# Performance work log

Hardware: AMD Instinct MI355X
Metric: run time of the kernel (lower is better)

Reference implementation:

```python
import jax, jax.numpy as jnp
import numpy as np

NH = 12
RD = 16  # partial RoPE dim


def setup_inputs() -> dict:
    key = jax.random.key(0)
    k1, k2, k3 = jax.random.split(key, 3)
    B, T, C = 4, 2048, 768
    x = jax.random.normal(k1, (B, T, C), dtype=jnp.float32)
    w_qkv = jax.random.normal(k2, (3 * C, C), dtype=jnp.float32) * 0.02
    w_out = jax.random.normal(k3, (C, C), dtype=jnp.float32) * 0.02
    return {"x": x, "w_qkv": w_qkv, "w_out": w_out}


def _rope_tables(T, dtype):
    freqs = 1.0 / (10000.0 ** (jnp.arange(0, RD, 2, dtype=jnp.float32) / RD))
    f = jnp.arange(T, dtype=jnp.float32)[:, None] * freqs[None, :]  # [T, RD//2]
    cos = jnp.cos(f)[None, None].astype(dtype)  # [1,1,T,RD//2]
    sin = jnp.sin(f)[None, None].astype(dtype)
    return cos, sin


def _rope(t, cos, sin):
    # t: [B, H, T, hd]; rotate only the first RD dims (split-half style)
    r, p = t[..., :RD], t[..., RD:]
    r1, r2 = r[..., : RD // 2], r[..., RD // 2 :]
    rot = jnp.concatenate([r1 * cos - r2 * sin, r2 * cos + r1 * sin], axis=-1)
    return jnp.concatenate([rot, p], axis=-1)


def reference(x, w_qkv, w_out):
    B, T, C = x.shape
    hd = C // NH
    qkv = jnp.einsum('btc,dc->btd', x, w_qkv).reshape(B, T, 3, NH, hd)
    q, k, v = (jnp.transpose(qkv[:, :, i], (0, 2, 1, 3)) for i in range(3))  # [B,H,T,hd]
    cos, sin = _rope_tables(T, x.dtype)
    q = _rope(q, cos, sin)
    k = _rope(k, cos, sin)
    scale = 1.0 / np.sqrt(hd).astype(np.float32)
    scores = jnp.einsum('bhqd,bhkd->bhqk', q, k) * scale  # [B,H,T,T]
    causal = jnp.tril(jnp.ones((T, T), dtype=bool))
    scores = jnp.where(causal[None, None], scores, jnp.finfo(scores.dtype).min)
    attn = jax.nn.softmax(scores, axis=-1)
    o = jnp.einsum('bhqk,bhkd->bhqd', attn, v)  # [B,H,T,hd]
    o = jnp.transpose(o, (0, 2, 1, 3)).reshape(B, T, C)
    return jnp.einsum('btc,dc->btd', o, w_out)
```

## Files before the change

### kernel.cpp

```cpp
#include <hip/hip_runtime.h>
#include <math.h>


namespace {

constexpr int B_ = 4, T_ = 2048, C_ = 768, NH_ = 12, HD_ = 64;
constexpr int BH_ = B_ * NH_;
constexpr size_t QS_ = (size_t)BH_ * T_ * HD_;

typedef short short8 __attribute__((ext_vector_type(8)));
typedef float f32x4 __attribute__((ext_vector_type(4)));

__device__ inline ushort f2bf(float f) {
    unsigned u = __builtin_bit_cast(unsigned, f);
    u += 0x7fff + ((u >> 16) & 1);
    return (ushort)(u >> 16);
}
__device__ inline float bf2f(ushort h) {
    unsigned u = (unsigned)h << 16;
    return __builtin_bit_cast(float, u);
}

__global__ __launch_bounds__(256) void cvt_bf16(const float4* __restrict__ a,
                                                ushort4* __restrict__ o, int n4)
{
    const int i = blockIdx.x * 256 + threadIdx.x;
    if (i >= n4) return;
    const float4 v = a[i];
    ushort4 u;
    u.x = f2bf(v.x); u.y = f2bf(v.y); u.z = f2bf(v.z); u.w = f2bf(v.w);
    o[i] = u;
}

template <int EPI>
__global__ __launch_bounds__(256) void mgemm(
    const ushort* __restrict__ A, const ushort* __restrict__ Bw,
    float* __restrict__ out, int K, int N_,
    ushort* __restrict__ qb, ushort* __restrict__ kb, ushort* __restrict__ vb)
{
    constexpr int BM = 128, BN = 128, BK = 32;
    __shared__ ushort As[BM * BK];
    __shared__ ushort Bs[BN * BK];

    const int tid = threadIdx.x;
    const int w = tid >> 6, l = tid & 63;
    const int lg = l >> 4, lc = l & 15;
    const int wr = w >> 1, wc = w & 1;
    const int m0 = blockIdx.y * BM;
    const int n0 = blockIdx.x * BN;

    f32x4 acc[4][4] = {};

    for (int k0 = 0; k0 < K; k0 += BK) {
#pragma unroll
        for (int i = 0; i < 2; ++i) {
            const int cb = w * 128 + i * 64;
            const int c = cb + l;
            const ushort* ga = &A[(size_t)(m0 + (c >> 2)) * K + k0 + (c & 3) * 8];
            const ushort* gb = &Bw[(size_t)(n0 + (c >> 2)) * K + k0 + (c & 3) * 8];
            __builtin_amdgcn_global_load_lds(
                (const __attribute__((address_space(1))) void*)ga,
                (__attribute__((address_space(3))) void*)&As[(size_t)cb * 8], 16, 0, 0);
            __builtin_amdgcn_global_load_lds(
                (const __attribute__((address_space(1))) void*)gb,
                (__attribute__((address_space(3))) void*)&Bs[(size_t)cb * 8], 16, 0, 0);
        }
        __syncthreads();

        short8 af[4], bf[4];
#pragma unroll
        for (int mi = 0; mi < 4; ++mi)
            af[mi] = *(const short8*)&As[(wr * 64 + mi * 16 + lc) * 32 + lg * 8];
#pragma unroll
        for (int nj = 0; nj < 4; ++nj)
            bf[nj] = *(const short8*)&Bs[(wc * 64 + nj * 16 + lc) * 32 + lg * 8];
#pragma unroll
        for (int mi = 0; mi < 4; ++mi)
#pragma unroll
            for (int nj = 0; nj < 4; ++nj)
                acc[mi][nj] = __builtin_amdgcn_mfma_f32_16x16x32_bf16(
                    af[mi], bf[nj], acc[mi][nj], 0, 0, 0);
        __syncthreads();
    }

    if constexpr (EPI == 0) {
        (void)qb; (void)kb; (void)vb;
#pragma unroll
        for (int mi = 0; mi < 4; ++mi) {
            const int m = m0 + wr * 64 + mi * 16 + lg * 4;
#pragma unroll
            for (int nj = 0; nj < 4; ++nj) {
                const int n = n0 + wc * 64 + nj * 16 + lc;
#pragma unroll
                for (int r = 0; r < 4; ++r)
                    out[(size_t)(m + r) * N_ + n] = acc[mi][nj][r];
            }
        }
    } else {
        (void)out; (void)N_;
#pragma unroll
        for (int mi = 0; mi < 4; ++mi) {
            const int m = m0 + wr * 64 + mi * 16 + lg * 4;
            const int b = m >> 11, t0 = m & (T_ - 1);
#pragma unroll
            for (int nj = 0; nj < 4; ++nj) {
                const int n = n0 + wc * 64 + nj * 16 + lc;
                const int sec = n / C_;
                const int cc = n - sec * C_;
                const int h = cc >> 6, di = cc & 63;
                if (sec == 2) {
                    ushort4 w4;
                    w4.x = f2bf(acc[mi][nj][0]); w4.y = f2bf(acc[mi][nj][1]);
                    w4.z = f2bf(acc[mi][nj][2]); w4.w = f2bf(acc[mi][nj][3]);
                    *(ushort4*)&vb[((size_t)(b * NH_ + h) * HD_ + di) * T_ + t0] = w4;
                } else {
                    ushort* dst = (sec == 0) ? qb : kb;
                    const float s = (sec == 0) ? 0.125f : 1.f;
#pragma unroll
                    for (int r = 0; r < 4; ++r)
                        dst[((size_t)(b * NH_ + h) * T_ + t0 + r) * HD_ + di] =
                            f2bf(acc[mi][nj][r] * s);
                }
            }
        }
    }
}

__global__ __launch_bounds__(256) void rope_kernel(ushort* __restrict__ q,
                                                   ushort* __restrict__ k)
{
    const int g = blockIdx.x * 256 + threadIdx.x;
    const int i = g & 7;
    int row = g >> 3;
    ushort* buf = q;
    if (row >= BH_ * T_) { buf = k; row -= BH_ * T_; }
    const int t = row & (T_ - 1);
    const float freq = __expf(-(float)i * 1.15129254649702f);
    const float a = (float)t * freq;
    const float c = cosf(a), s = sinf(a);
    ushort* p = buf + (size_t)row * HD_;
    const float r1 = bf2f(p[i]), r2 = bf2f(p[i + 8]);
    p[i]     = f2bf(r1 * c - r2 * s);
    p[i + 8] = f2bf(r2 * c + r1 * s);
}

__global__ __launch_bounds__(256) void flash_mfma(
    const ushort* __restrict__ q, const ushort* __restrict__ k,
    const ushort* __restrict__ v, ushort* __restrict__ o)
{
    __shared__ ushort Ks[64 * 64];
    __shared__ ushort Vs[64 * 64];
    __shared__ ushort Ps[4][16 * 64];

    const int qi = ((int)blockIdx.x + (int)blockIdx.y) & 31;
    const int q0 = qi * 64;
    const int bh = blockIdx.y;
    const int b = bh / NH_, h = bh % NH_;
    const int tid = threadIdx.x;
    const int w = tid >> 6, l = tid & 63;
    const int lg = l >> 4, lc = l & 15;

    const size_t kvbase = (size_t)bh * T_ * HD_;
    const size_t vbase  = (size_t)bh * HD_ * T_;

    short8 aq[2];
    {
        const ushort* qp = q + kvbase + (size_t)(q0 + w * 16 + lc) * HD_ + lg * 8;
        aq[0] = *(const short8*)(qp);
        aq[1] = *(const short8*)(qp + 32);
    }

    f32x4 oa[4] = {};
    float m[4], lr[4];
#pragma unroll
    for (int r = 0; r < 4; ++r) { m[r] = -1e30f; lr[r] = 0.f; }

    const int nkt = qi + 1;
    for (int t0i = 0; t0i < nkt; ++t0i) {
        const int t0 = t0i * 64;
        __syncthreads();
#pragma unroll
        for (int i = 0; i < 2; ++i) {
            const int cb = (w * 2 + i) * 64;
            const int c = cb + l;
            const int row = c >> 3, s8 = (c & 7) * 8;
            const int col = s8 ^ ((row & 7) << 3);
            __builtin_amdgcn_global_load_lds(
                (const __attribute__((address_space(1))) void*)
                    &k[kvbase + (size_t)(t0 + row) * HD_ + col],
                (__attribute__((address_space(3))) void*)&Ks[cb * 8], 16, 0, 0);
            __builtin_amdgcn_global_load_lds(
                (const __attribute__((address_space(1))) void*)
                    &v[vbase + (size_t)row * T_ + t0 + col],
                (__attribute__((address_space(3))) void*)&Vs[cb * 8], 16, 0, 0);
        }
        __syncthreads();

        f32x4 sa[4];
        __builtin_amdgcn_s_setprio(1);
#pragma unroll
        for (int kc = 0; kc < 4; ++kc) {
            const int row = kc * 16 + lc;
            const int base = row * 64;
            const int sw = (row & 7) << 3;
            short8 b0 = *(const short8*)&Ks[(base + lg * 8) ^ sw];
            short8 b1 = *(const short8*)&Ks[(base + 32 + lg * 8) ^ sw];
            f32x4 z = {0.f, 0.f, 0.f, 0.f};
            z = __builtin_amdgcn_mfma_f32_16x16x32_bf16(aq[0], b0, z, 0, 0, 0);
            z = __builtin_amdgcn_mfma_f32_16x16x32_bf16(aq[1], b1, z, 0, 0, 0);
            sa[kc] = z;
        }
        __builtin_amdgcn_s_setprio(0);

        if (t0 + 63 > q0 + w * 16) {
#pragma unroll
            for (int kc = 0; kc < 4; ++kc) {
                const int kg = t0 + kc * 16 + lc;
#pragma unroll
                for (int r = 0; r < 4; ++r) {
                    const int qg = q0 + w * 16 + lg * 4 + r;
                    if (kg > qg) sa[kc][r] = -1e30f;
                }
            }
        }

        float sc[4];
#pragma unroll
        for (int r = 0; r < 4; ++r) {
            float a = fmaxf(fmaxf(sa[0][r], sa[1][r]), fmaxf(sa[2][r], sa[3][r]));
            a = fmaxf(a, __shfl_xor(a, 1));
            a = fmaxf(a, __shfl_xor(a, 2));
            a = fmaxf(a, __shfl_xor(a, 4));
            a = fmaxf(a, __shfl_xor(a, 8));
            const float mn = fmaxf(m[r], a);
            sc[r] = __expf(m[r] - mn);
            m[r] = mn;
        }
#pragma unroll
        for (int r = 0; r < 4; ++r) {
            lr[r] *= sc[r];
            oa[0][r] *= sc[r]; oa[1][r] *= sc[r];
            oa[2][r] *= sc[r]; oa[3][r] *= sc[r];
        }
        float ls[4] = {0.f, 0.f, 0.f, 0.f};
#pragma unroll
        for (int kc = 0; kc < 4; ++kc) {
#pragma unroll
            for (int r = 0; r < 4; ++r) {
                const float p = __expf(sa[kc][r] - m[r]);
                ls[r] += p;
                const int qr = lg * 4 + r;
                Ps[w][(qr * 64 + kc * 16 + lc) ^ ((qr & 7) << 3)] = f2bf(p);
            }
        }
#pragma unroll
        for (int r = 0; r < 4; ++r) {
            float a = ls[r];
            a += __shfl_xor(a, 1); a += __shfl_xor(a, 2);
            a += __shfl_xor(a, 4); a += __shfl_xor(a, 8);
            lr[r] += a;
        }

        short8 pa[2];
        {
            const int sw = (lc & 7) << 3;
            pa[0] = *(const short8*)&Ps[w][(lc * 64 + lg * 8) ^ sw];
            pa[1] = *(const short8*)&Ps[w][(lc * 64 + 32 + lg * 8) ^ sw];
        }
        __builtin_amdgcn_s_setprio(1);
#pragma unroll
        for (int dc = 0; dc < 4; ++dc) {
            const int row = dc * 16 + lc;
            const int base = row * 64;
            const int sw = (row & 7) << 3;
            short8 b0 = *(const short8*)&Vs[(base + lg * 8) ^ sw];
            short8 b1 = *(const short8*)&Vs[(base + 32 + lg * 8) ^ sw];
            oa[dc] = __builtin_amdgcn_mfma_f32_16x16x32_bf16(pa[0], b0, oa[dc], 0, 0, 0);
            oa[dc] = __builtin_amdgcn_mfma_f32_16x16x32_bf16(pa[1], b1, oa[dc], 0, 0, 0);
        }
        __builtin_amdgcn_s_setprio(0);
    }

#pragma unroll
    for (int r = 0; r < 4; ++r) {
        const float inv = 1.f / lr[r];
        const int qg = q0 + w * 16 + lg * 4 + r;
        ushort* op = o + (size_t)(b * T_ + qg) * C_ + h * HD_ + lc;
#pragma unroll
        for (int dc = 0; dc < 4; ++dc) op[dc * 16] = f2bf(oa[dc][r] * inv);
    }
}

}

extern "C" void kernel_launch(void* const* d_in, const int* in_sizes, int n_in,
                              void* d_out, int out_size, void* d_ws, size_t ws_size,
                              hipStream_t stream)
{
    (void)in_sizes; (void)n_in; (void)out_size; (void)ws_size;
    const float* x     = (const float*)d_in[0];
    const float* w_qkv = (const float*)d_in[1];
    const float* w_out = (const float*)d_in[2];
    float* out = (float*)d_out;

    ushort* xb    = (ushort*)d_ws;
    ushort* wqkvb = xb + QS_;
    ushort* woutb = wqkvb + (size_t)3 * C_ * C_;
    ushort* qb    = woutb + (size_t)C_ * C_;
    ushort* kb    = qb + QS_;
    ushort* vb    = kb + QS_;
    ushort* ob    = vb + QS_;

    cvt_bf16<<<6144, 256, 0, stream>>>((const float4*)x, (ushort4*)xb, 1572864);
    cvt_bf16<<<1728, 256, 0, stream>>>((const float4*)w_qkv, (ushort4*)wqkvb, 442368);
    cvt_bf16<<<576, 256, 0, stream>>>((const float4*)w_out, (ushort4*)woutb, 147456);

    mgemm<1><<<dim3(18, 64), 256, 0, stream>>>(xb, wqkvb, nullptr, C_, 0, qb, kb, vb);

    rope_kernel<<<6144, 256, 0, stream>>>(qb, kb);

    flash_mfma<<<dim3(T_ / 64, BH_), 256, 0, stream>>>(qb, kb, vb, ob);

    mgemm<0><<<dim3(6, 64), 256, 0, stream>>>(ob, woutb, out, C_, C_,
                                              nullptr, nullptr, nullptr);
}
```

Measured before the change: 290.6 us.

## Double-buffer K/V tiles, pair causal query blocks per workgroup, merge conversion launches

The flash attention kernel now uses double-buffered K/V shared memory. The next tile is prefetched with global_load_lds while the current tile is computed, and the prefetch runs across the boundary between the two query segments. Each workgroup handles query block j and then 31-j, which balances causal work and halves the grid. Softmax switches to exp2f with log2(e) folded into the Q scale, and the three fp32-to-bf16 conversion launches become a single kernel. This doubles K/V LDS use and relies on only one barrier per iteration to order buffer reuse.

```diff
diff --git a/kernel.cpp b/kernel.cpp
--- a/kernel.cpp
+++ b/kernel.cpp
@@ -21,15 +21,20 @@
     return __builtin_bit_cast(float, u);
 }
 
-__global__ __launch_bounds__(256) void cvt_bf16(const float4* __restrict__ a,
-                                                ushort4* __restrict__ o, int n4)
-{
-    const int i = blockIdx.x * 256 + threadIdx.x;
-    if (i >= n4) return;
-    const float4 v = a[i];
+__global__ __launch_bounds__(256) void cvt_all(
+    const float4* __restrict__ x, const float4* __restrict__ wq,
+    const float4* __restrict__ wo, ushort4* __restrict__ xb,
+    ushort4* __restrict__ wqb, ushort4* __restrict__ wob)
+{
+    int i = blockIdx.x * 256 + threadIdx.x;
+    const float4* s; ushort4* d;
+    if (i < 1572864) { s = x; d = xb; }
+    else if (i < 2015232) { s = wq; d = wqb; i -= 1572864; }
+    else { s = wo; d = wob; i -= 2015232; if (i >= 147456) return; }
+    const float4 v = s[i];
     ushort4 u;
     u.x = f2bf(v.x); u.y = f2bf(v.y); u.z = f2bf(v.z); u.w = f2bf(v.w);
-    o[i] = u;
+    d[i] = u;
 }
 
 template <int EPI>
@@ -115,7 +120,7 @@
                     *(ushort4*)&vb[((size_t)(b * NH_ + h) * HD_ + di) * T_ + t0] = w4;
                 } else {
                     ushort* dst = (sec == 0) ? qb : kb;
-                    const float s = (sec == 0) ? 0.125f : 1.f;
+                    const float s = (sec == 0) ? 0.18033688f : 1.f;
 #pragma unroll
                     for (int r = 0; r < 4; ++r)
                         dst[((size_t)(b * NH_ + h) * T_ + t0 + r) * HD_ + di] =
@@ -148,12 +153,11 @@
     const ushort* __restrict__ q, const ushort* __restrict__ k,
     const ushort* __restrict__ v, ushort* __restrict__ o)
 {
-    __shared__ ushort Ks[64 * 64];
-    __shared__ ushort Vs[64 * 64];
+    __shared__ ushort Ks[2][64 * 64];
+    __shared__ ushort Vs[2][64 * 64];
     __shared__ ushort Ps[4][16 * 64];
 
-    const int qi = ((int)blockIdx.x + (int)blockIdx.y) & 31;
-    const int q0 = qi * 64;
+    const int j = blockIdx.x;
     const int bh = blockIdx.y;
     const int b = bh / NH_, h = bh % NH_;
     const int tid = threadIdx.x;
@@ -163,22 +167,7 @@
     const size_t kvbase = (size_t)bh * T_ * HD_;
     const size_t vbase  = (size_t)bh * HD_ * T_;
 
-    short8 aq[2];
-    {
-        const ushort* qp = q + kvbase + (size_t)(q0 + w * 16 + lc) * HD_ + lg * 8;
-        aq[0] = *(const short8*)(qp);
-        aq[1] = *(const short8*)(qp + 32);
-    }
-
-    f32x4 oa[4] = {};
-    float m[4], lr[4];
-#pragma unroll
-    for (int r = 0; r < 4; ++r) { m[r] = -1e30f; lr[r] = 0.f; }
-
-    const int nkt = qi + 1;
-    for (int t0i = 0; t0i < nkt; ++t0i) {
-        const int t0 = t0i * 64;
-        __syncthreads();
+    auto stage = [&](int buf, int t0) {
 #pragma unroll
         for (int i = 0; i < 2; ++i) {
             const int cb = (w * 2 + i) * 64;
@@ -188,106 +177,138 @@
             __builtin_amdgcn_global_load_lds(
                 (const __attribute__((address_space(1))) void*)
                     &k[kvbase + (size_t)(t0 + row) * HD_ + col],
-                (__attribute__((address_space(3))) void*)&Ks[cb * 8], 16, 0, 0);
+                (__attribute__((address_space(3))) void*)&Ks[buf][cb * 8], 16, 0, 0);
             __builtin_amdgcn_global_load_lds(
                 (const __attribute__((address_space(1))) void*)
                     &v[vbase + (size_t)row * T_ + t0 + col],
-                (__attribute__((address_space(3))) void*)&Vs[cb * 8], 16, 0, 0);
-        }
-        __syncthreads();
-
-        f32x4 sa[4];
-        __builtin_amdgcn_s_setprio(1);
-#pragma unroll
-        for (int kc = 0; kc < 4; ++kc) {
-            const int row = kc * 16 + lc;
-            const int base = row * 64;
-            const int sw = (row & 7) << 3;
-            short8 b0 = *(const short8*)&Ks[(base + lg * 8) ^ sw];
-            short8 b1 = *(const short8*)&Ks[(base + 32 + lg * 8) ^ sw];
-            f32x4 z = {0.f, 0.f, 0.f, 0.f};
-            z = __builtin_amdgcn_mfma_f32_16x16x32_bf16(aq[0], b0, z, 0, 0, 0);
-            z = __builtin_amdgcn_mfma_f32_16x16x32_bf16(aq[1], b1, z, 0, 0, 0);
-            sa[kc] = z;
-        }
-        __builtin_amdgcn_s_setprio(0);
-
-        if (t0 + 63 > q0 + w * 16) {
+                (__attribute__((address_space(3))) void*)&Vs[buf][cb * 8], 16, 0, 0);
+        }
+    };
+
+    int cur = 0;
+    stage(0, 0);
+
+    for (int seg = 0; seg < 2; ++seg) {
+        const int qi = seg ? (31 - j) : j;
+        const int q0 = qi * 64;
+
+        short8 aq[2];
+        {
+            const ushort* qp =
+                q + kvbase + (size_t)(q0 + w * 16 + lc) * HD_ + lg * 8;
+            aq[0] = *(const short8*)(qp);
+            aq[1] = *(const short8*)(qp + 32);
+        }
+        f32x4 oa[4] = {};
+        float m[4], lr[4];
+#pragma unroll
+        for (int r = 0; r < 4; ++r) { m[r] = -1e30f; lr[r] = 0.f; }
+
+        const int nkt = qi + 1;
+        for (int t0i = 0; t0i < nkt; ++t0i) {
+            const int t0 = t0i * 64;
+            __syncthreads();
+            const bool lastAll = (seg == 1) && (t0i == nkt - 1);
+            if (!lastAll) {
+                const int nt0 = (t0i + 1 < nkt) ? (t0 + 64) : 0;
+                stage(cur ^ 1, nt0);
+            }
+
+            f32x4 sa[4];
+            __builtin_amdgcn_s_setprio(1);
 #pragma unroll
             for (int kc = 0; kc < 4; ++kc) {
-                const int kg = t0 + kc * 16 + lc;
+                const int row = kc * 16 + lc;
+                const int base = row * 64;
+                const int sw = (row & 7) << 3;
+                short8 b0 = *(const short8*)&Ks[cur][(base + lg * 8) ^ sw];
+                short8 b1 = *(const short8*)&Ks[cur][(base + 32 + lg * 8) ^ sw];
+                f32x4 z = {0.f, 0.f, 0.f, 0.f};
+                z = __builtin_amdgcn_mfma_f32_16x16x32_bf16(aq[0], b0, z, 0, 0, 0);
+                z = __builtin_amdgcn_mfma_f32_16x16x32_bf16(aq[1], b1, z, 0, 0, 0);
+                sa[kc] = z;
+            }
+            __builtin_amdgcn_s_setprio(0);
+
+            if (t0 + 63 > q0 + w * 16) {
+#pragma unroll
+                for (int kc = 0; kc < 4; ++kc) {
+                    const int kg = t0 + kc * 16 + lc;
+#pragma unroll
+                    for (int r = 0; r < 4; ++r) {
+                        const int qg = q0 + w * 16 + lg * 4 + r;
+                        if (kg > qg) sa[kc][r] = -1e30f;
+                    }
+                }
+            }
+
+            float sc[4];
+#pragma unroll
+            for (int r = 0; r < 4; ++r) {
+                float a = fmaxf(fmaxf(sa[0][r], sa[1][r]),
+                                fmaxf(sa[2][r], sa[3][r]));
+                a = fmaxf(a, __shfl_xor(a, 1));
+                a = fmaxf(a, __shfl_xor(a, 2));
+                a = fmaxf(a, __shfl_xor(a, 4));
+                a = fmaxf(a, __shfl_xor(a, 8));
+                const float mn = fmaxf(m[r], a);
+                sc[r] = exp2f(m[r] - mn);
+                m[r] = mn;
+            }
+#pragma unroll
+            for (int r = 0; r < 4; ++r) {
+                lr[r] *= sc[r];
+                oa[0][r] *= sc[r]; oa[1][r] *= sc[r];
+                oa[2][r] *= sc[r]; oa[3][r] *= sc[r];
+            }
+            float ls[4] = {0.f, 0.f, 0.f, 0.f};
+#pragma unroll
+            for (int kc = 0; kc < 4; ++kc) {
 #pragma unroll
                 for (int r = 0; r < 4; ++r) {
-                    const int qg = q0 + w * 16 + lg * 4 + r;
-                    if (kg > qg) sa[kc][r] = -1e30f;
+                    const float p = exp2f(sa[kc][r] - m[r]);
+                    ls[r] += p;
+                    const int qr = lg * 4 + r;
+                    Ps[w][(qr * 64 + kc * 16 + lc) ^ ((qr & 7) << 3)] = f2bf(p);
                 }
             }
-        }
-
-        float sc[4];
+#pragma unroll
+            for (int r = 0; r < 4; ++r) {
+                float a = ls[r];
+                a += __shfl_xor(a, 1); a += __shfl_xor(a, 2);
+                a += __shfl_xor(a, 4); a += __shfl_xor(a, 8);
+                lr[r] += a;
+            }
+
+            short8 pa[2];
+            {
+                const int sw = (lc & 7) << 3;
+                pa[0] = *(const short8*)&Ps[w][(lc * 64 + lg * 8) ^ sw];
+                pa[1] = *(const short8*)&Ps[w][(lc * 64 + 32 + lg * 8) ^ sw];
+            }
+            __builtin_amdgcn_s_setprio(1);
+#pragma unroll
+            for (int dc = 0; dc < 4; ++dc) {
+                const int row = dc * 16 + lc;
+                const int base = row * 64;
+                const int sw = (row & 7) << 3;
+                short8 b0 = *(const short8*)&Vs[cur][(base + lg * 8) ^ sw];
+                short8 b1 = *(const short8*)&Vs[cur][(base + 32 + lg * 8) ^ sw];
+                oa[dc] = __builtin_amdgcn_mfma_f32_16x16x32_bf16(pa[0], b0, oa[dc], 0, 0, 0);
+                oa[dc] = __builtin_amdgcn_mfma_f32_16x16x32_bf16(pa[1], b1, oa[dc], 0, 0, 0);
+            }
+            __builtin_amdgcn_s_setprio(0);
+            cur ^= 1;
+        }
+
 #pragma unroll
         for (int r = 0; r < 4; ++r) {
-            float a = fmaxf(fmaxf(sa[0][r], sa[1][r]), fmaxf(sa[2][r], sa[3][r]));
-            a = fmaxf(a, __shfl_xor(a, 1));
-            a = fmaxf(a, __shfl_xor(a, 2));
-            a = fmaxf(a, __shfl_xor(a, 4));
-            a = fmaxf(a, __shfl_xor(a, 8));
-            const float mn = fmaxf(m[r], a);
-            sc[r] = __expf(m[r] - mn);
-            m[r] = mn;
-        }
-#pragma unroll
-        for (int r = 0; r < 4; ++r) {
-            lr[r] *= sc[r];
-            oa[0][r] *= sc[r]; oa[1][r] *= sc[r];
-            oa[2][r] *= sc[r]; oa[3][r] *= sc[r];
-        }
-        float ls[4] = {0.f, 0.f, 0.f, 0.f};
-#pragma unroll
-        for (int kc = 0; kc < 4; ++kc) {
-#pragma unroll
-            for (int r = 0; r < 4; ++r) {
-                const float p = __expf(sa[kc][r] - m[r]);
-                ls[r] += p;
-                const int qr = lg * 4 + r;
-                Ps[w][(qr * 64 + kc * 16 + lc) ^ ((qr & 7) << 3)] = f2bf(p);
-            }
-        }
-#pragma unroll
-        for (int r = 0; r < 4; ++r) {
-            float a = ls[r];
-            a += __shfl_xor(a, 1); a += __shfl_xor(a, 2);
-            a += __shfl_xor(a, 4); a += __shfl_xor(a, 8);
-            lr[r] += a;
-        }
-
-        short8 pa[2];
-        {
-            const int sw = (lc & 7) << 3;
-            pa[0] = *(const short8*)&Ps[w][(lc * 64 + lg * 8) ^ sw];
-            pa[1] = *(const short8*)&Ps[w][(lc * 64 + 32 + lg * 8) ^ sw];
-        }
-        __builtin_amdgcn_s_setprio(1);
-#pragma unroll
-        for (int dc = 0; dc < 4; ++dc) {
-            const int row = dc * 16 + lc;
-            const int base = row * 64;
-            const int sw = (row & 7) << 3;
-            short8 b0 = *(const short8*)&Vs[(base + lg * 8) ^ sw];
-            short8 b1 = *(const short8*)&Vs[(base + 32 + lg * 8) ^ sw];
-            oa[dc] = __builtin_amdgcn_mfma_f32_16x16x32_bf16(pa[0], b0, oa[dc], 0, 0, 0);
-            oa[dc] = __builtin_amdgcn_mfma_f32_16x16x32_bf16(pa[1], b1, oa[dc], 0, 0, 0);
-        }
-        __builtin_amdgcn_s_setprio(0);
-    }
-
-#pragma unroll
-    for (int r = 0; r < 4; ++r) {
-        const float inv = 1.f / lr[r];
-        const int qg = q0 + w * 16 + lg * 4 + r;
-        ushort* op = o + (size_t)(b * T_ + qg) * C_ + h * HD_ + lc;
-#pragma unroll
-        for (int dc = 0; dc < 4; ++dc) op[dc * 16] = f2bf(oa[dc][r] * inv);
+            const float inv = 1.f / lr[r];
+            const int qg = q0 + w * 16 + lg * 4 + r;
+            ushort* op = o + (size_t)(b * T_ + qg) * C_ + h * HD_ + lc;
+#pragma unroll
+            for (int dc = 0; dc < 4; ++dc) op[dc * 16] = f2bf(oa[dc][r] * inv);
+        }
     }
 }
 
@@ -311,15 +332,15 @@
     ushort* vb    = kb + QS_;
     ushort* ob    = vb + QS_;
 
-    cvt_bf16<<<6144, 256, 0, stream>>>((const float4*)x, (ushort4*)xb, 1572864);
-    cvt_bf16<<<1728, 256, 0, stream>>>((const float4*)w_qkv, (ushort4*)wqkvb, 442368);
-    cvt_bf16<<<576, 256, 0, stream>>>((const float4*)w_out, (ushort4*)woutb, 147456);
+    cvt_all<<<8448, 256, 0, stream>>>((const float4*)x, (const float4*)w_qkv,
+                                      (const float4*)w_out, (ushort4*)xb,
+                                      (ushort4*)wqkvb, (ushort4*)woutb);
 
     mgemm<1><<<dim3(18, 64), 256, 0, stream>>>(xb, wqkvb, nullptr, C_, 0, qb, kb, vb);
 
     rope_kernel<<<6144, 256, 0, stream>>>(qb, kb);
 
-    flash_mfma<<<dim3(T_ / 64, BH_), 256, 0, stream>>>(qb, kb, vb, ob);
+    flash_mfma<<<dim3(16, BH_), 256, 0, stream>>>(qb, kb, vb, ob);
 
     mgemm<0><<<dim3(6, 64), 256, 0, stream>>>(ob, woutb, out, C_, C_,
                                               nullptr, nullptr, nullptr);
```

Result: faster. 262.1 us (-9.8%).
